# Optimization experiments

Measured on AMD Instinct MI355X. Metric: run time of the kernel, lower is better.

Reference implementation:

```python
import jax, jax.numpy as jnp
import numpy as np

P = 16  # patch size
D = 768  # embedding dim


def setup_inputs() -> dict:
    key = jax.random.key(0)
    k_img, k_w, k_b = jax.random.split(key, 3)
    B, H, W, C = 64, 224, 224, 3
    image = jax.random.normal(k_img, (B, H, W, C), dtype=jnp.float32)
    patch_dim = P * P * C  # 768
    # Keras Dense default: glorot_uniform kernel, zeros bias
    limit = np.sqrt(6.0 / (patch_dim + D)).astype(np.float32)
    W_proj = jax.random.uniform(k_w, (patch_dim, D), dtype=jnp.float32,
                                minval=-limit, maxval=limit)
    b_proj = jnp.zeros((D,), dtype=jnp.float32)
    return {"image": image, "W_proj": W_proj, "b_proj": b_proj}


def reference(image, W_proj, b_proj):
    B, H, W, C = image.shape
    nh, nw = H // P, W // P
    # Fused im2col replacing the per-patch slicing loop:
    # [B,H,W,C] -> [B, nh, P, nw, P, C] -> [B, nh, nw, P, P, C] -> [B, nh*nw, P*P*C]
    # Row-major (p_i, p_j) patch order matches the original nested loop, and
    # flatten of a [B,P,P,C] slice matches the (P,P,C) raveling here.
    patches = image.reshape(B, nh, P, nw, P, C)
    patches = patches.transpose(0, 1, 3, 2, 4, 5).reshape(B, nh * nw, P * P * C)
    # Dense + exact GELU (tf.keras.activations.gelu default approximate=False)
    x = jnp.einsum('bnp,pd->bnd', patches, W_proj) + b_proj
    return jax.nn.gelu(x, approximate=False)
```

## Files before the change

### kernel.cpp

```cpp
#include <hip/hip_runtime.h>
#include <hip/hip_bf16.h>
#include <math.h>

#define MM 12544
#define KK 768
#define NN 768
#define BM 64
#define BN 256
#define BK 64
#define KT 12
#define MT 196
#define NT 3
#define TILE_A_BYTES (BM*BK*2)
#define TILE_B_BYTES (BN*BK*2)

#define IM2COL_BLOCKS ((MM * 96) / 256)
#define WTPACK_BLOCKS ((NN * 96) / 256)

typedef __bf16 v8bf __attribute__((ext_vector_type(8)));
typedef float  v4f  __attribute__((ext_vector_type(4)));

__global__ __launch_bounds__(256) void pack_kernel(const float* __restrict__ img,
                                                   const float* __restrict__ w,
                                                   __hip_bfloat16* __restrict__ apack,
                                                   __hip_bfloat16* __restrict__ wpack) {
    if (blockIdx.x < IM2COL_BLOCKS) {
        int tid = blockIdx.x * 256 + threadIdx.x;
        int gg  = tid % 96;
        int m   = tid / 96;
        int b   = m / 196;
        int pm  = m - b * 196;
        int pr  = pm / 14;
        int pc  = pm - pr * 14;
        int k0  = gg * 8;
        int i   = k0 / 48;
        int rem = k0 - i * 48;
        const float* src = img + (size_t)(((b * 224 + pr * 16 + i) * 224 + pc * 16) * 3 + rem);
        float4 f0 = *(const float4*)src;
        float4 f1 = *(const float4*)(src + 4);
        int mt = m >> 6;
        int r  = m & 63;
        int kt = gg >> 3;
        int g  = gg & 7;
        int gs = g ^ (r & 7);
        union { __hip_bfloat16 h[8]; uint4 u; } o;
        o.h[0] = __float2bfloat16(f0.x); o.h[1] = __float2bfloat16(f0.y);
        o.h[2] = __float2bfloat16(f0.z); o.h[3] = __float2bfloat16(f0.w);
        o.h[4] = __float2bfloat16(f1.x); o.h[5] = __float2bfloat16(f1.y);
        o.h[6] = __float2bfloat16(f1.z); o.h[7] = __float2bfloat16(f1.w);
        *(uint4*)(apack + ((size_t)(mt * KT + kt) * BM + r) * BK + gs * 8) = o.u;
    } else {
        int tid = (blockIdx.x - IM2COL_BLOCKS) * 256 + threadIdx.x;
        int n   = tid % 768;
        int gg  = tid / 768;
        int k0  = gg * 8;
        float f[8];
#pragma unroll
        for (int j = 0; j < 8; j++) f[j] = w[(size_t)(k0 + j) * NN + n];
        int nt = n >> 8;
        int nr = n & 255;
        int kt = gg >> 3;
        int g  = gg & 7;
        int gs = g ^ (nr & 7);
        union { __hip_bfloat16 h[8]; uint4 u; } o;
#pragma unroll
        for (int j = 0; j < 8; j++) o.h[j] = __float2bfloat16(f[j]);
        *(uint4*)(wpack + ((size_t)(nt * KT + kt) * BN + nr) * BK + gs * 8) = o.u;
    }
}

__device__ __forceinline__ float gelu_fast(float x) {
    float t2 = 1.5957691216057308f * x * (1.0f + 0.044715f * x * x);
    float e  = __expf(t2);
    float r  = __builtin_amdgcn_rcpf(e + 1.0f);
    return x - x * r;
}

__global__ __launch_bounds__(256, 3) void gemm_gelu(const __hip_bfloat16* __restrict__ apack,
                                                    const __hip_bfloat16* __restrict__ wpack,
                                                    const float* __restrict__ bias,
                                                    float* __restrict__ out) {
    __shared__ __align__(16) __hip_bfloat16 As[BM * BK];
    __shared__ __align__(16) __hip_bfloat16 Bs[BN * BK];

    const int blk = blockIdx.x;
    const int nt  = blk % 3;
    const int mt  = blk / 3;

    const int tid  = threadIdx.x;
    const int lane = tid & 63;
    const int wave = tid >> 6;
    const int wn   = wave * 64;
    const int col  = lane & 15;
    const int quad = lane >> 4;
    const int cl7  = col & 7;

    v4f acc[4][4];
    const v4f vzero = {0.f, 0.f, 0.f, 0.f};
#pragma unroll
    for (int a = 0; a < 4; a++)
#pragma unroll
        for (int c = 0; c < 4; c++) acc[a][c] = vzero;

    const char* aT = (const char*)apack + (size_t)mt * KT * TILE_A_BYTES;
    const char* bT = (const char*)wpack + (size_t)nt * KT * TILE_B_BYTES;

    for (int kt = 0; kt < KT; kt++) {
#pragma unroll
        for (int p = 0; p < 2; p++) {
            int off = p * 4096 + tid * 16;
            __builtin_amdgcn_global_load_lds(
                (const __attribute__((address_space(1))) void*)(aT + off),
                (__attribute__((address_space(3))) void*)((char*)As + off), 16, 0, 0);
        }
#pragma unroll
        for (int p = 0; p < 8; p++) {
            int off = p * 4096 + tid * 16;
            __builtin_amdgcn_global_load_lds(
                (const __attribute__((address_space(1))) void*)(bT + off),
                (__attribute__((address_space(3))) void*)((char*)Bs + off), 16, 0, 0);
        }
        aT += TILE_A_BYTES;
        bT += TILE_B_BYTES;
        __syncthreads();

#pragma unroll
        for (int ks = 0; ks < 2; ks++) {
            const int gs = (ks * 4 + quad) ^ cl7;
            const v8bf* pa = (const v8bf*)(As + col * BK + gs * 8);
            const v8bf* pb = (const v8bf*)(Bs + (wn + col) * BK + gs * 8);
            v8bf af[4], bfr[4];
#pragma unroll
            for (int mi = 0; mi < 4; mi++) af[mi] = pa[mi * 128];
#pragma unroll
            for (int ni = 0; ni < 4; ni++) bfr[ni] = pb[ni * 128];
#pragma unroll
            for (int mi = 0; mi < 4; mi++)
#pragma unroll
                for (int ni = 0; ni < 4; ni++)
                    acc[mi][ni] = __builtin_amdgcn_mfma_f32_16x16x32_bf16(
                        af[mi], bfr[ni], acc[mi][ni], 0, 0, 0);
        }
        __syncthreads();
    }

#pragma unroll
    for (int ni = 0; ni < 4; ni++) {
        int n    = nt * BN + wn + ni * 16 + col;
        float bv = bias[n];
#pragma unroll
        for (int mi = 0; mi < 4; mi++) {
            int rowb = mt * BM + mi * 16 + quad * 4;
            float* po = out + (size_t)rowb * NN + n;
#pragma unroll
            for (int rg = 0; rg < 4; rg++) {
                float x = acc[mi][ni][rg] + bv;
                po[(size_t)rg * NN] = gelu_fast(x);
            }
        }
    }
}

extern "C" void kernel_launch(void* const* d_in, const int* in_sizes, int n_in,
                              void* d_out, int out_size, void* d_ws, size_t ws_size,
                              hipStream_t stream) {
    const float* img   = (const float*)d_in[0];
    const float* wproj = (const float*)d_in[1];
    const float* bias  = (const float*)d_in[2];
    float* out = (float*)d_out;

    __hip_bfloat16* apack = (__hip_bfloat16*)d_ws;
    __hip_bfloat16* wpack = (__hip_bfloat16*)((char*)d_ws + (size_t)MM * KK * 2);

    pack_kernel<<<dim3(IM2COL_BLOCKS + WTPACK_BLOCKS), dim3(256), 0, stream>>>(
        img, wproj, apack, wpack);
    gemm_gelu<<<dim3(MT * NT), dim3(256), 0, stream>>>(apack, wpack, bias, out);
}
```

Before: 117.8 us.

## Fuse im2col and bf16 conversion of image into GEMM A-tile loading

Removes the separate im2col pack of the image into a bf16 workspace buffer. The GEMM kernel now reads fp32 image patches directly with float4 loads, converts them to bf16 and writes them into the swizzled LDS tile. This drops one full write and read of the packed activation matrix. In exchange, each image tile is re-read by the three N-tile blocks in fp32, and the A loads become synchronous register loads rather than direct global-to-LDS loads.

```diff
diff --git a/kernel.cpp b/kernel.cpp
--- a/kernel.cpp
+++ b/kernel.cpp
@@ -11,62 +11,31 @@
 #define KT 12
 #define MT 196
 #define NT 3
-#define TILE_A_BYTES (BM*BK*2)
 #define TILE_B_BYTES (BN*BK*2)
 
-#define IM2COL_BLOCKS ((MM * 96) / 256)
 #define WTPACK_BLOCKS ((NN * 96) / 256)
 
 typedef __bf16 v8bf __attribute__((ext_vector_type(8)));
 typedef float  v4f  __attribute__((ext_vector_type(4)));
 
-__global__ __launch_bounds__(256) void pack_kernel(const float* __restrict__ img,
-                                                   const float* __restrict__ w,
-                                                   __hip_bfloat16* __restrict__ apack,
-                                                   __hip_bfloat16* __restrict__ wpack) {
-    if (blockIdx.x < IM2COL_BLOCKS) {
-        int tid = blockIdx.x * 256 + threadIdx.x;
-        int gg  = tid % 96;
-        int m   = tid / 96;
-        int b   = m / 196;
-        int pm  = m - b * 196;
-        int pr  = pm / 14;
-        int pc  = pm - pr * 14;
-        int k0  = gg * 8;
-        int i   = k0 / 48;
-        int rem = k0 - i * 48;
-        const float* src = img + (size_t)(((b * 224 + pr * 16 + i) * 224 + pc * 16) * 3 + rem);
-        float4 f0 = *(const float4*)src;
-        float4 f1 = *(const float4*)(src + 4);
-        int mt = m >> 6;
-        int r  = m & 63;
-        int kt = gg >> 3;
-        int g  = gg & 7;
-        int gs = g ^ (r & 7);
-        union { __hip_bfloat16 h[8]; uint4 u; } o;
-        o.h[0] = __float2bfloat16(f0.x); o.h[1] = __float2bfloat16(f0.y);
-        o.h[2] = __float2bfloat16(f0.z); o.h[3] = __float2bfloat16(f0.w);
-        o.h[4] = __float2bfloat16(f1.x); o.h[5] = __float2bfloat16(f1.y);
-        o.h[6] = __float2bfloat16(f1.z); o.h[7] = __float2bfloat16(f1.w);
-        *(uint4*)(apack + ((size_t)(mt * KT + kt) * BM + r) * BK + gs * 8) = o.u;
-    } else {
-        int tid = (blockIdx.x - IM2COL_BLOCKS) * 256 + threadIdx.x;
-        int n   = tid % 768;
-        int gg  = tid / 768;
-        int k0  = gg * 8;
-        float f[8];
+__global__ __launch_bounds__(256) void wt_pack(const float* __restrict__ w,
+                                               __hip_bfloat16* __restrict__ wpack) {
+    int tid = blockIdx.x * 256 + threadIdx.x;
+    int n   = tid % 768;
+    int gg  = tid / 768;
+    int k0  = gg * 8;
+    float f[8];
 #pragma unroll
-        for (int j = 0; j < 8; j++) f[j] = w[(size_t)(k0 + j) * NN + n];
-        int nt = n >> 8;
-        int nr = n & 255;
-        int kt = gg >> 3;
-        int g  = gg & 7;
-        int gs = g ^ (nr & 7);
-        union { __hip_bfloat16 h[8]; uint4 u; } o;
+    for (int j = 0; j < 8; j++) f[j] = w[(size_t)(k0 + j) * NN + n];
+    int nt = n >> 8;
+    int nr = n & 255;
+    int kt = gg >> 3;
+    int g  = gg & 7;
+    int gs = g ^ (nr & 7);
+    union { __hip_bfloat16 h[8]; uint4 u; } o;
 #pragma unroll
-        for (int j = 0; j < 8; j++) o.h[j] = __float2bfloat16(f[j]);
-        *(uint4*)(wpack + ((size_t)(nt * KT + kt) * BN + nr) * BK + gs * 8) = o.u;
-    }
+    for (int j = 0; j < 8; j++) o.h[j] = __float2bfloat16(f[j]);
+    *(uint4*)(wpack + ((size_t)(nt * KT + kt) * BN + nr) * BK + gs * 8) = o.u;
 }
 
 __device__ __forceinline__ float gelu_fast(float x) {
@@ -76,7 +45,7 @@
     return x - x * r;
 }
 
-__global__ __launch_bounds__(256, 3) void gemm_gelu(const __hip_bfloat16* __restrict__ apack,
+__global__ __launch_bounds__(256, 3) void gemm_gelu(const float* __restrict__ img,
                                                     const __hip_bfloat16* __restrict__ wpack,
                                                     const float* __restrict__ bias,
                                                     float* __restrict__ out) {
@@ -95,6 +64,18 @@
     const int quad = lane >> 4;
     const int cl7  = col & 7;
 
+    const int r = tid >> 2;
+    const int q = tid & 3;
+    unsigned m  = (unsigned)(mt * BM + r);
+    unsigned b  = m / 196u;
+    unsigned pm = m - b * 196u;
+    unsigned pr = pm / 14u;
+    unsigned pc = pm - pr * 14u;
+    const float* pbase = img + (size_t)(((b * 224u + pr * 16u) * 224u + pc * 16u) * 3u);
+    const int gs0 = (2 * q) ^ (r & 7);
+    const int gs1 = gs0 ^ 1;
+    uint4* As16 = (uint4*)As;
+
     v4f acc[4][4];
     const v4f vzero = {0.f, 0.f, 0.f, 0.f};
 #pragma unroll
@@ -102,17 +83,9 @@
 #pragma unroll
         for (int c = 0; c < 4; c++) acc[a][c] = vzero;
 
-    const char* aT = (const char*)apack + (size_t)mt * KT * TILE_A_BYTES;
     const char* bT = (const char*)wpack + (size_t)nt * KT * TILE_B_BYTES;
 
     for (int kt = 0; kt < KT; kt++) {
-#pragma unroll
-        for (int p = 0; p < 2; p++) {
-            int off = p * 4096 + tid * 16;
-            __builtin_amdgcn_global_load_lds(
-                (const __attribute__((address_space(1))) void*)(aT + off),
-                (__attribute__((address_space(3))) void*)((char*)As + off), 16, 0, 0);
-        }
 #pragma unroll
         for (int p = 0; p < 8; p++) {
             int off = p * 4096 + tid * 16;
@@ -120,8 +93,28 @@
                 (const __attribute__((address_space(1))) void*)(bT + off),
                 (__attribute__((address_space(3))) void*)((char*)Bs + off), 16, 0, 0);
         }
-        aT += TILE_A_BYTES;
         bT += TILE_B_BYTES;
+
+        float4 f4[4];
+#pragma unroll
+        for (int j = 0; j < 4; j++) {
+            unsigned k   = (unsigned)(kt * 64 + q * 16 + j * 4);
+            unsigned i   = k / 48u;
+            unsigned rem = k - i * 48u;
+            f4[j] = *(const float4*)(pbase + i * 672u + rem);
+        }
+        union { __hip_bfloat16 h[8]; uint4 u; } lo, hi;
+        lo.h[0] = __float2bfloat16(f4[0].x); lo.h[1] = __float2bfloat16(f4[0].y);
+        lo.h[2] = __float2bfloat16(f4[0].z); lo.h[3] = __float2bfloat16(f4[0].w);
+        lo.h[4] = __float2bfloat16(f4[1].x); lo.h[5] = __float2bfloat16(f4[1].y);
+        lo.h[6] = __float2bfloat16(f4[1].z); lo.h[7] = __float2bfloat16(f4[1].w);
+        hi.h[0] = __float2bfloat16(f4[2].x); hi.h[1] = __float2bfloat16(f4[2].y);
+        hi.h[2] = __float2bfloat16(f4[2].z); hi.h[3] = __float2bfloat16(f4[2].w);
+        hi.h[4] = __float2bfloat16(f4[3].x); hi.h[5] = __float2bfloat16(f4[3].y);
+        hi.h[6] = __float2bfloat16(f4[3].z); hi.h[7] = __float2bfloat16(f4[3].w);
+        As16[r * 8 + gs0] = lo.u;
+        As16[r * 8 + gs1] = hi.u;
+
         __syncthreads();
 
 #pragma unroll
@@ -169,10 +162,8 @@
     const float* bias  = (const float*)d_in[2];
     float* out = (float*)d_out;
 
-    __hip_bfloat16* apack = (__hip_bfloat16*)d_ws;
-    __hip_bfloat16* wpack = (__hip_bfloat16*)((char*)d_ws + (size_t)MM * KK * 2);
+    __hip_bfloat16* wpack = (__hip_bfloat16*)d_ws;
 
-    pack_kernel<<<dim3(IM2COL_BLOCKS + WTPACK_BLOCKS), dim3(256), 0, stream>>>(
-        img, wproj, apack, wpack);
-    gemm_gelu<<<dim3(MT * NT), dim3(256), 0, stream>>>(apack, wpack, bias, out);
+    wt_pack<<<dim3(WTPACK_BLOCKS), dim3(256), 0, stream>>>(wproj, wpack);
+    gemm_gelu<<<dim3(MT * NT), dim3(256), 0, stream>>>(img, wpack, bias, out);
 }
```

New measurement: 124.5 us. 1.06x slower.
